# Kernel optimization log

Measured on AMD Instinct MI355X. Metric: run time of the kernel, lower is better.

## Reference

```python
import jax, jax.numpy as jnp
import numpy as np

B = 131072
NQ = 5
Z = jnp.array([1.0, -1.0], dtype=jnp.float32)


def _axshape(w):
    return [2 if k == w else 1 for k in range(NQ)]


def _apply_1q(state, U, w):
    # state: (B,2,2,2,2,2) complex64; apply 2x2 gate U on qubit w
    st = jnp.moveaxis(state, 1 + w, -1)
    st = st @ U.T
    return jnp.moveaxis(st, -1, 1 + w)


def _rx(t):
    c = jnp.cos(t / 2)
    s = jnp.sin(t / 2)
    return jnp.stack([jnp.stack([c + 0j, -1j * s]), jnp.stack([-1j * s, c + 0j])]).astype(jnp.complex64)


def _ry(t):
    c = jnp.cos(t / 2)
    s = jnp.sin(t / 2)
    return jnp.stack([jnp.stack([c, -s]), jnp.stack([s, c])]).astype(jnp.complex64)


def _quantum(comb, rw):
    # comb: (B,4). Wires 0,1 <- short feats, wire 2 <- 0, wires 3,4 <- long feats.
    zero = jnp.zeros_like(comb[:, 0])
    angles = [comb[:, 0], comb[:, 1], zero, comb[:, 2], comb[:, 3]]
    # RY(a)|0> = [cos(a/2), sin(a/2)] -> batched product state via einsum (B,32)
    qs = [jnp.stack([jnp.cos(a / 2), jnp.sin(a / 2)], -1).astype(jnp.complex64) for a in angles]
    state = jnp.einsum('bi,bj,bk,bl,bm->bijklm', *qs)
    for layer in range(3):
        for i in range(NQ):
            state = _apply_1q(state, _rx(rw[layer, i, 0]), i)
            state = _apply_1q(state, _ry(rw[layer, i, 1]), i)
        for i in range(NQ):
            for j in range(i + 1, NQ):
                # CNOT(i,j) RZ(th,j) CNOT(i,j) == exp(-i th/2 Z_i Z_j): diagonal phase
                zz = Z.reshape(_axshape(i)) * Z.reshape(_axshape(j))
                phase = jnp.exp((-0.5j) * rw[layer, i, j].astype(jnp.complex64) * zz.astype(jnp.complex64))
                state = state * phase[None]
    probs = jnp.real(state * jnp.conj(state))
    ez = [jnp.sum(probs * Z.reshape(_axshape(w))[None], axis=(1, 2, 3, 4, 5)) for w in range(NQ)]
    return jnp.stack(ez, -1)  # (B,5)


def _forward(x_short, x_long, conv_s_w, conv_s_b, lin_s_w, lin_s_b, conv_l_w, conv_l_b, lin_l_w, lin_l_b, reservoir_weights, readout_w, readout_b):
    dn = ('NCH', 'OIH', 'NCH')
    h = jax.lax.conv_general_dilated(x_short, conv_s_w, (1,), [(1, 1)], dimension_numbers=dn) + conv_s_b[None, :, None]
    feat_s = jax.nn.relu(h).reshape(h.shape[0], -1) @ lin_s_w.T + lin_s_b  # (B,2)
    h = jax.lax.conv_general_dilated(x_long, conv_l_w, (1,), [(2, 2)], dimension_numbers=dn) + conv_l_b[None, :, None]
    h = jax.nn.relu(h)
    h = h.reshape(h.shape[0], 4, 10, 2).max(-1)  # MaxPool1d(2): 20 -> 10
    feat_l = h.reshape(h.shape[0], -1) @ lin_l_w.T + lin_l_b  # (B,2)
    comb = jnp.concatenate([feat_s, feat_l], axis=1)  # (B,4)
    qz = _quantum(comb, reservoir_weights)  # (B,5)
    return qz @ readout_w.T + readout_b  # (B,1)


def setup_inputs() -> dict:
    key = jax.random.key(0)
    ks = jax.random.split(key, 12)
    f32 = jnp.float32
    return {
        'x_short': jax.random.normal(ks[0], (B, 1, 5), f32),
        'x_long': jax.random.normal(ks[1], (B, 1, 20), f32),
        'conv_s_w': jax.random.normal(ks[2], (4, 1, 3), f32) * 0.3,
        'conv_s_b': jax.random.normal(ks[3], (4,), f32) * 0.1,
        'lin_s_w': jax.random.normal(ks[4], (2, 20), f32) * 0.15,
        'lin_s_b': jnp.zeros((2,), f32),
        'conv_l_w': jax.random.normal(ks[5], (4, 1, 5), f32) * 0.3,
        'conv_l_b': jax.random.normal(ks[6], (4,), f32) * 0.1,
        'lin_l_w': jax.random.normal(ks[7], (2, 40), f32) * 0.1,
        'lin_l_b': jnp.zeros((2,), f32),
        'reservoir_weights': jax.random.normal(ks[8], (3, 5, 5), f32),
        'readout_w': jax.random.normal(ks[9], (1, 5), f32) * 0.3,
        'readout_b': jnp.zeros((1,), f32),
    }


def reference(x_short, x_long, conv_s_w, conv_s_b, lin_s_w, lin_s_b, conv_l_w, conv_l_b, lin_l_w, lin_l_b, reservoir_weights, readout_w, readout_b):
    return _forward(x_short, x_long, conv_s_w, conv_s_b, lin_s_w, lin_s_b, conv_l_w, conv_l_b, lin_l_w, lin_l_b, reservoir_weights, readout_w, readout_b)
```

## Files before the change

### kernel.cpp

```cpp
#include <hip/hip_runtime.h>
#include <math.h>


__global__ __launch_bounds__(256) void qcr_kernel(
    const float* __restrict__ x_short, const float* __restrict__ x_long,
    const float* __restrict__ conv_s_w, const float* __restrict__ conv_s_b,
    const float* __restrict__ lin_s_w,  const float* __restrict__ lin_s_b,
    const float* __restrict__ conv_l_w, const float* __restrict__ conv_l_b,
    const float* __restrict__ lin_l_w,  const float* __restrict__ lin_l_b,
    const float* __restrict__ rw,       const float* __restrict__ readout_w,
    const float* __restrict__ readout_b, float* __restrict__ out, int nb)
{
    __shared__ float s_rxc[15], s_rxs[15], s_ryc[15], s_rys[15];
    __shared__ float s_zzc[96], s_zzs[96], s_coef[32];

    const int tid = threadIdx.x;

    if (tid < 15) {
        const int l = tid / 5, i = tid % 5;
        const float tx = rw[l*25 + i*5 + 0] * 0.5f;
        const float ty = rw[l*25 + i*5 + 1] * 0.5f;
        s_rxc[tid] = cosf(tx); s_rxs[tid] = sinf(tx);
        s_ryc[tid] = cosf(ty); s_rys[tid] = sinf(ty);
    }
    if (tid >= 32 && tid < 128) {
        const int e = tid - 32;
        const int l = e >> 5, bi = e & 31;
        float ang = 0.f;
        for (int i = 0; i < 5; ++i) {
            const float si = ((bi >> (4 - i)) & 1) ? -1.f : 1.f;
            for (int j = i + 1; j < 5; ++j) {
                const float sj = ((bi >> (4 - j)) & 1) ? -1.f : 1.f;
                ang += rw[l*25 + i*5 + j] * si * sj;
            }
        }
        ang *= -0.5f;
        s_zzc[e] = cosf(ang); s_zzs[e] = sinf(ang);
    }
    if (tid >= 128 && tid < 160) {
        const int bi = tid - 128;
        float c = 0.f;
        for (int w = 0; w < 5; ++w) {
            const float sw = ((bi >> (4 - w)) & 1) ? -1.f : 1.f;
            c += readout_w[w] * sw;
        }
        s_coef[bi] = c;
    }
    __syncthreads();

    const int b = blockIdx.x * 256 + tid;
    if (b >= nb) return;

    float xs[5];
    #pragma unroll
    for (int p = 0; p < 5; ++p) xs[p] = x_short[b*5 + p];

    float f0 = lin_s_b[0], f1 = lin_s_b[1];
    #pragma unroll
    for (int c = 0; c < 4; ++c) {
        #pragma unroll
        for (int p = 0; p < 5; ++p) {
            float h = conv_s_b[c];
            #pragma unroll
            for (int k = 0; k < 3; ++k) {
                const int q = p - 1 + k;
                if (q >= 0 && q < 5) h += conv_s_w[c*3 + k] * xs[q];
            }
            h = fmaxf(h, 0.f);
            f0 += lin_s_w[      c*5 + p] * h;
            f1 += lin_s_w[20 + c*5 + p] * h;
        }
    }

    float xl[20];
    #pragma unroll
    for (int p = 0; p < 20; ++p) xl[p] = x_long[b*20 + p];

    float g0 = lin_l_b[0], g1 = lin_l_b[1];
    #pragma unroll
    for (int c = 0; c < 4; ++c) {
        #pragma unroll
        for (int q = 0; q < 10; ++q) {
            float hm = 0.f;
            #pragma unroll
            for (int t = 0; t < 2; ++t) {
                const int p = 2*q + t;
                float h = conv_l_b[c];
                #pragma unroll
                for (int k = 0; k < 5; ++k) {
                    const int u = p - 2 + k;
                    if (u >= 0 && u < 20) h += conv_l_w[c*5 + k] * xl[u];
                }
                hm = fmaxf(hm, h);
            }
            g0 += lin_l_w[      c*10 + q] * hm;
            g1 += lin_l_w[40 + c*10 + q] * hm;
        }
    }

    float p0c, p0s, p1c, p1s, p3c, p3s, p4c, p4s;
    sincosf(f0 * 0.5f, &p0s, &p0c);
    sincosf(f1 * 0.5f, &p1s, &p1c);
    sincosf(g0 * 0.5f, &p3s, &p3c);
    sincosf(g1 * 0.5f, &p4s, &p4c);

    float ar[32], ai[32];
    #pragma unroll
    for (int idx = 0; idx < 32; ++idx) {
        float v;
        if ((idx >> 2) & 1) {
            v = 0.f;
        } else {
            v = ((idx >> 4) & 1 ? p0s : p0c)
              * ((idx >> 3) & 1 ? p1s : p1c)
              * ((idx >> 1) & 1 ? p3s : p3c)
              * ((idx      ) & 1 ? p4s : p4c);
        }
        ar[idx] = v; ai[idx] = 0.f;
    }

    for (int l = 0; l < 3; ++l) {
        #pragma unroll
        for (int qb = 0; qb < 5; ++qb) {
            const float rc = s_rxc[l*5 + qb], rs = s_rxs[l*5 + qb];
            const float yc = s_ryc[l*5 + qb], ys = s_rys[l*5 + qb];
            const int str = 1 << (4 - qb);
            #pragma unroll
            for (int g = 0; g < 16; ++g) {
                const int i0 = ((g & ~(str - 1)) << 1) | (g & (str - 1));
                const int i1 = i0 | str;
                const float a0r = ar[i0], a0i = ai[i0];
                const float a1r = ar[i1], a1i = ai[i1];
                const float n0r =  rc*a0r + rs*a1i;
                const float n0i =  rc*a0i - rs*a1r;
                const float n1r =  rs*a0i + rc*a1r;
                const float n1i = -rs*a0r + rc*a1i;
                ar[i0] = yc*n0r - ys*n1r;
                ai[i0] = yc*n0i - ys*n1i;
                ar[i1] = ys*n0r + yc*n1r;
                ai[i1] = ys*n0i + yc*n1i;
            }
        }
        #pragma unroll
        for (int idx = 0; idx < 32; ++idx) {
            const float pc = s_zzc[l*32 + idx], ps = s_zzs[l*32 + idx];
            const float r = ar[idx]*pc - ai[idx]*ps;
            ai[idx]       = ar[idx]*ps + ai[idx]*pc;
            ar[idx]       = r;
        }
    }

    float acc = readout_b[0];
    #pragma unroll
    for (int idx = 0; idx < 32; ++idx)
        acc += (ar[idx]*ar[idx] + ai[idx]*ai[idx]) * s_coef[idx];
    out[b] = acc;
}

extern "C" void kernel_launch(void* const* d_in, const int* in_sizes, int n_in,
                              void* d_out, int out_size, void* d_ws, size_t ws_size,
                              hipStream_t stream) {
    const float* x_short    = (const float*)d_in[0];
    const float* x_long     = (const float*)d_in[1];
    const float* conv_s_w   = (const float*)d_in[2];
    const float* conv_s_b   = (const float*)d_in[3];
    const float* lin_s_w    = (const float*)d_in[4];
    const float* lin_s_b    = (const float*)d_in[5];
    const float* conv_l_w   = (const float*)d_in[6];
    const float* conv_l_b   = (const float*)d_in[7];
    const float* lin_l_w    = (const float*)d_in[8];
    const float* lin_l_b    = (const float*)d_in[9];
    const float* rw         = (const float*)d_in[10];
    const float* readout_w  = (const float*)d_in[11];
    const float* readout_b  = (const float*)d_in[12];
    float* out = (float*)d_out;

    const int nb = in_sizes[0] / 5;
    dim3 grid((nb + 255) / 256), block(256);
    hipLaunchKernelGGL(qcr_kernel, grid, block, 0, stream,
                       x_short, x_long, conv_s_w, conv_s_b, lin_s_w, lin_s_b,
                       conv_l_w, conv_l_b, lin_l_w, lin_l_b, rw, readout_w,
                       readout_b, out, nb);
}
```

Measured before the change: 99.87 us.

## Precompute quantum circuit as trigonometric polynomial coefficients in a prep kernel

Because the circuit is linear in the input product state, the output is a quadratic form in the four encoding amplitudes. A single-block prep kernel simulates the circuit on the 16 basis states and builds the 16x16 observable matrix. It then converts that matrix into 81 Fourier coefficients in cos/sin of the full angles. The main kernel now only evaluates this tensor polynomial per sample instead of running a 32-amplitude complex statevector simulation. It also loads x_long with float4, which relies on each 80-byte row being 16-byte aligned. The cost is an extra kernel launch that runs serially before the main kernel.

```diff
diff --git a/kernel.cpp b/kernel.cpp
--- a/kernel.cpp
+++ b/kernel.cpp
@@ -2,17 +2,15 @@
 #include <math.h>
 
 
-__global__ __launch_bounds__(256) void qcr_kernel(
-    const float* __restrict__ x_short, const float* __restrict__ x_long,
-    const float* __restrict__ conv_s_w, const float* __restrict__ conv_s_b,
-    const float* __restrict__ lin_s_w,  const float* __restrict__ lin_s_b,
-    const float* __restrict__ conv_l_w, const float* __restrict__ conv_l_b,
-    const float* __restrict__ lin_l_w,  const float* __restrict__ lin_l_b,
-    const float* __restrict__ rw,       const float* __restrict__ readout_w,
-    const float* __restrict__ readout_b, float* __restrict__ out, int nb)
+__global__ __launch_bounds__(256) void qcr_prep(
+    const float* __restrict__ rw, const float* __restrict__ readout_w,
+    const float* __restrict__ readout_b, float* __restrict__ Dout)
 {
     __shared__ float s_rxc[15], s_rxs[15], s_ryc[15], s_rys[15];
     __shared__ float s_zzc[96], s_zzs[96], s_coef[32];
+    __shared__ float phir[16][33], phii[16][33];
+    __shared__ float sA[16][16];
+    __shared__ float sC[81];
 
     const int tid = threadIdx.x;
 
@@ -48,7 +46,114 @@
     }
     __syncthreads();
 
-    const int b = blockIdx.x * 256 + tid;
+    if (tid < 16) {
+        float ar[32], ai[32];
+        const int P = ((tid & 12) << 1) | (tid & 3);
+        #pragma unroll
+        for (int idx = 0; idx < 32; ++idx) { ar[idx] = (idx == P) ? 1.f : 0.f; ai[idx] = 0.f; }
+
+        for (int l = 0; l < 3; ++l) {
+            #pragma unroll
+            for (int qb = 0; qb < 5; ++qb) {
+                const float rc = s_rxc[l*5 + qb], rs = s_rxs[l*5 + qb];
+                const float yc = s_ryc[l*5 + qb], ys = s_rys[l*5 + qb];
+                const int str = 1 << (4 - qb);
+                #pragma unroll
+                for (int g = 0; g < 16; ++g) {
+                    const int i0 = ((g & ~(str - 1)) << 1) | (g & (str - 1));
+                    const int i1 = i0 | str;
+                    const float a0r = ar[i0], a0i = ai[i0];
+                    const float a1r = ar[i1], a1i = ai[i1];
+                    const float n0r =  rc*a0r + rs*a1i;
+                    const float n0i =  rc*a0i - rs*a1r;
+                    const float n1r =  rs*a0i + rc*a1r;
+                    const float n1i = -rs*a0r + rc*a1i;
+                    ar[i0] = yc*n0r - ys*n1r;
+                    ai[i0] = yc*n0i - ys*n1i;
+                    ar[i1] = ys*n0r + yc*n1r;
+                    ai[i1] = ys*n0i + yc*n1i;
+                }
+            }
+            #pragma unroll
+            for (int idx = 0; idx < 32; ++idx) {
+                const float pc = s_zzc[l*32 + idx], ps = s_zzs[l*32 + idx];
+                const float r = ar[idx]*pc - ai[idx]*ps;
+                ai[idx]       = ar[idx]*ps + ai[idx]*pc;
+                ar[idx]       = r;
+            }
+        }
+        #pragma unroll
+        for (int k = 0; k < 32; ++k) { phir[tid][k] = ar[k]; phii[tid][k] = ai[k]; }
+    }
+    __syncthreads();
+
+    {
+        const int p = tid >> 4, q = tid & 15;
+        float acc = 0.f;
+        #pragma unroll
+        for (int k = 0; k < 32; ++k)
+            acc += s_coef[k] * (phir[p][k]*phir[q][k] + phii[p][k]*phii[q][k]);
+        sA[p][q] = acc;
+    }
+    __syncthreads();
+
+    if (tid < 81) {
+        const int j0 = tid / 27, j1 = (tid / 9) % 3, j3 = (tid / 3) % 3, j4 = tid % 3;
+        const int n0 = 1 + (j0 == 1), n1 = 1 + (j1 == 1);
+        const int n3 = 1 + (j3 == 1), n4 = 1 + (j4 == 1);
+        float s = 0.f;
+        for (int a0 = 0; a0 < n0; ++a0) {
+            const int pb0 = (j0 == 2) ? 1 : ((j0 == 1) ? a0 : 0);
+            const int qb0 = (j0 == 0) ? 0 : ((j0 == 1) ? 1 - a0 : 1);
+            for (int a1 = 0; a1 < n1; ++a1) {
+                const int pb1 = (j1 == 2) ? 1 : ((j1 == 1) ? a1 : 0);
+                const int qb1 = (j1 == 0) ? 0 : ((j1 == 1) ? 1 - a1 : 1);
+                for (int a3 = 0; a3 < n3; ++a3) {
+                    const int pb3 = (j3 == 2) ? 1 : ((j3 == 1) ? a3 : 0);
+                    const int qb3 = (j3 == 0) ? 0 : ((j3 == 1) ? 1 - a3 : 1);
+                    for (int a4 = 0; a4 < n4; ++a4) {
+                        const int pb4 = (j4 == 2) ? 1 : ((j4 == 1) ? a4 : 0);
+                        const int qb4 = (j4 == 0) ? 0 : ((j4 == 1) ? 1 - a4 : 1);
+                        s += sA[(pb0<<3)|(pb1<<2)|(pb3<<1)|pb4]
+                               [(qb0<<3)|(qb1<<2)|(qb3<<1)|qb4];
+                    }
+                }
+            }
+        }
+        sC[tid] = s;
+    }
+    __syncthreads();
+
+    #pragma unroll
+    for (int pass = 0; pass < 4; ++pass) {
+        const int P  = (pass == 0) ? 27 : (pass == 1) ? 9 : (pass == 2) ? 3 : 1;
+        const int O1 = (pass == 0) ? 9  : 27;
+        const int O2 = (pass <= 1) ? 3  : 9;
+        const int O3 = (pass <= 2) ? 1  : 3;
+        if (tid < 27) {
+            const int base = (tid / 9) * O1 + ((tid / 3) % 3) * O2 + (tid % 3) * O3;
+            const float v0 = sC[base], v1 = sC[base + P], v2 = sC[base + 2*P];
+            sC[base]       = 0.5f * (v0 + v2);
+            sC[base + P]   = 0.5f * (v0 - v2);
+            sC[base + 2*P] = 0.5f * v1;
+        }
+        __syncthreads();
+    }
+
+    if (tid == 0) sC[0] += readout_b[0];
+    __syncthreads();
+    if (tid < 81) Dout[tid] = sC[tid];
+}
+
+__global__ __launch_bounds__(256) void qcr_main(
+    const float* __restrict__ x_short, const float* __restrict__ x_long,
+    const float* __restrict__ conv_s_w, const float* __restrict__ conv_s_b,
+    const float* __restrict__ lin_s_w,  const float* __restrict__ lin_s_b,
+    const float* __restrict__ conv_l_w, const float* __restrict__ conv_l_b,
+    const float* __restrict__ lin_l_w,  const float* __restrict__ lin_l_b,
+    const float* __restrict__ D, float* __restrict__ out, int nb)
+{
+    const int b = blockIdx.x * 256 + threadIdx.x;
     if (b >= nb) return;
 
     float xs[5];
@@ -73,8 +178,14 @@
     }
 
     float xl[20];
-    #pragma unroll
-    for (int p = 0; p < 20; ++p) xl[p] = x_long[b*20 + p];
+    {
+        const float4* xl4 = reinterpret_cast<const float4*>(x_long + b*20);
+        #pragma unroll
+        for (int v = 0; v < 5; ++v) {
+            const float4 t = xl4[v];
+            xl[4*v+0] = t.x; xl[4*v+1] = t.y; xl[4*v+2] = t.z; xl[4*v+3] = t.w;
+        }
+    }
 
     float g0 = lin_l_b[0], g1 = lin_l_b[1];
     #pragma unroll
@@ -98,63 +209,26 @@
         }
     }
 
-    float p0c, p0s, p1c, p1s, p3c, p3s, p4c, p4s;
-    sincosf(f0 * 0.5f, &p0s, &p0c);
-    sincosf(f1 * 0.5f, &p1s, &p1c);
-    sincosf(g0 * 0.5f, &p3s, &p3c);
-    sincosf(g1 * 0.5f, &p4s, &p4c);
-
-    float ar[32], ai[32];
-    #pragma unroll
-    for (int idx = 0; idx < 32; ++idx) {
-        float v;
-        if ((idx >> 2) & 1) {
-            v = 0.f;
-        } else {
-            v = ((idx >> 4) & 1 ? p0s : p0c)
-              * ((idx >> 3) & 1 ? p1s : p1c)
-              * ((idx >> 1) & 1 ? p3s : p3c)
-              * ((idx      ) & 1 ? p4s : p4c);
-        }
-        ar[idx] = v; ai[idx] = 0.f;
-    }
-
-    for (int l = 0; l < 3; ++l) {
-        #pragma unroll
-        for (int qb = 0; qb < 5; ++qb) {
-            const float rc = s_rxc[l*5 + qb], rs = s_rxs[l*5 + qb];
-            const float yc = s_ryc[l*5 + qb], ys = s_rys[l*5 + qb];
-            const int str = 1 << (4 - qb);
-            #pragma unroll
-            for (int g = 0; g < 16; ++g) {
-                const int i0 = ((g & ~(str - 1)) << 1) | (g & (str - 1));
-                const int i1 = i0 | str;
-                const float a0r = ar[i0], a0i = ai[i0];
-                const float a1r = ar[i1], a1i = ai[i1];
-                const float n0r =  rc*a0r + rs*a1i;
-                const float n0i =  rc*a0i - rs*a1r;
-                const float n1r =  rs*a0i + rc*a1r;
-                const float n1i = -rs*a0r + rc*a1i;
-                ar[i0] = yc*n0r - ys*n1r;
-                ai[i0] = yc*n0i - ys*n1i;
-                ar[i1] = ys*n0r + yc*n1r;
-                ai[i1] = ys*n0i + yc*n1i;
-            }
-        }
-        #pragma unroll
-        for (int idx = 0; idx < 32; ++idx) {
-            const float pc = s_zzc[l*32 + idx], ps = s_zzs[l*32 + idx];
-            const float r = ar[idx]*pc - ai[idx]*ps;
-            ai[idx]       = ar[idx]*ps + ai[idx]*pc;
-            ar[idx]       = r;
-        }
-    }
-
-    float acc = readout_b[0];
-    #pragma unroll
-    for (int idx = 0; idx < 32; ++idx)
-        acc += (ar[idx]*ar[idx] + ai[idx]*ai[idx]) * s_coef[idx];
-    out[b] = acc;
+    float C0, S0, C1, S1, C3, S3, C4, S4;
+    sincosf(f0, &S0, &C0);
+    sincosf(f1, &S1, &C1);
+    sincosf(g0, &S3, &C3);
+    sincosf(g1, &S4, &C4);
+
+    float t4[27];
+    #pragma unroll
+    for (int j = 0; j < 27; ++j)
+        t4[j] = D[3*j] + C4 * D[3*j + 1] + S4 * D[3*j + 2];
+    float t3[9];
+    #pragma unroll
+    for (int j = 0; j < 9; ++j)
+        t3[j] = t4[3*j] + C3 * t4[3*j + 1] + S3 * t4[3*j + 2];
+    float t1[3];
+    #pragma unroll
+    for (int j = 0; j < 3; ++j)
+        t1[j] = t3[3*j] + C1 * t3[3*j + 1] + S1 * t3[3*j + 2];
+
+    out[b] = t1[0] + C0 * t1[1] + S0 * t1[2];
 }
 
 extern "C" void kernel_launch(void* const* d_in, const int* in_sizes, int n_in,
@@ -174,11 +248,13 @@
     const float* readout_w  = (const float*)d_in[11];
     const float* readout_b  = (const float*)d_in[12];
     float* out = (float*)d_out;
+    float* Dws = (float*)d_ws;
 
     const int nb = in_sizes[0] / 5;
-    dim3 grid((nb + 255) / 256), block(256);
-    hipLaunchKernelGGL(qcr_kernel, grid, block, 0, stream,
+
+    hipLaunchKernelGGL(qcr_prep, dim3(1), dim3(256), 0, stream,
+                       rw, readout_w, readout_b, Dws);
+    hipLaunchKernelGGL(qcr_main, dim3((nb + 255) / 256), dim3(256), 0, stream,
                        x_short, x_long, conv_s_w, conv_s_b, lin_s_w, lin_s_b,
-                       conv_l_w, conv_l_b, lin_l_w, lin_l_b, rw, readout_w,
-                       readout_b, out, nb);
+                       conv_l_w, conv_l_b, lin_l_w, lin_l_b, Dws, out, nb);
 }
```

Result: no change. 100.2 us (+0.3%).
